# Kernel optimization log

Measured on AMD Instinct MI355X. Metric: run time of the kernel, lower is better.

The kernel has to match this reference:

```python
import jax, jax.numpy as jnp
import numpy as np

D_HEAD = 64  # module's self.heads scaling constant


def setup_inputs() -> dict:
    key = jax.random.key(0)
    kq, kk, kv = jax.random.split(key, 3)
    N, HW, C = 4, 4096, 64
    Q = jax.random.normal(kq, (N, HW, C), dtype=jnp.float32)
    K = jax.random.normal(kk, (N, HW, C), dtype=jnp.float32)
    V = jax.random.normal(kv, (N, HW, C), dtype=jnp.float32)
    return {"Q": Q, "K": K, "V": V}


def reference(Q, K, V):
    # logits[n, q, k] = Q[n,q,:] . K[n,k,:] / sqrt(d_head)
    scale = 1.0 / jnp.sqrt(jnp.asarray(D_HEAD, dtype=Q.dtype))
    logits = jnp.einsum("nqc,nkc->nqk", Q, K) * scale  # [N, HW, HW]
    # NOTE: softmax over the QUERY axis (dim=1), non-standard
    attn = jax.nn.softmax(logits, axis=1)
    return jnp.einsum("nqk,nkc->nqc", attn, V)
```

## Files before the change

kernel.cpp:

```cpp
#include <hip/hip_runtime.h>
#include <hip/hip_bf16.h>

#define NB 4
#define HWN 4096
#define CD 64
#define NSTRIDE (HWN * CD)

typedef short short8 __attribute__((ext_vector_type(8), may_alias));
typedef short short4v __attribute__((ext_vector_type(4), may_alias));
typedef float f32x4 __attribute__((ext_vector_type(4), may_alias));
typedef unsigned int uint4v __attribute__((ext_vector_type(4), may_alias));

__device__ constexpr float C1 = 0.18033688011112042f;

__device__ __forceinline__ unsigned short f2bf(float f) {
    unsigned u = __builtin_bit_cast(unsigned, f);
    u = (u + 0x7FFFu + ((u >> 16) & 1u)) >> 16;
    return (unsigned short)u;
}

__device__ __forceinline__ float fexp2(float x) {
#if __has_builtin(__builtin_amdgcn_exp2f)
    return __builtin_amdgcn_exp2f(x);
#else
    return exp2f(x);
#endif
}

__device__ __forceinline__ unsigned pk2(float a, float b) {
    __hip_bfloat162 h = __float22bfloat162_rn(float2{a, b});
    unsigned u;
    __builtin_memcpy(&u, &h, 4);
    return u;
}

__device__ __forceinline__ size_t qk_swz(int row, int c) {
    return (size_t)(row >> 4) * 1024 + (c >> 5) * 512 +
           ((((c >> 3) & 3) * 16 + (row & 15)) * 8) + (c & 7);
}

__device__ __forceinline__ int k_perm_row(int r) {
    int G = r >> 5, a = r & 31;
    int j = a & 7, g = a >> 3;
    return (G << 5) + ((j >> 2) << 4) + g * 4 + (j & 3);
}

__global__ __launch_bounds__(256) void cvt_qkv(const float* __restrict__ Q,
                                               const float* __restrict__ K,
                                               const float* __restrict__ V,
                                               unsigned short* __restrict__ Qs,
                                               unsigned short* __restrict__ Ks,
                                               unsigned short* __restrict__ Vts,
                                               float* __restrict__ l) {
    __shared__ float tile[64][65];
    int tid = threadIdx.x;
    if (blockIdx.x < 16) {
        int zi = blockIdx.x * 256 + tid;
        *(f32x4*)(l + (size_t)zi * 4) = f32x4{0.f, 0.f, 0.f, 0.f};
    }
    {
        int i = (blockIdx.x * 256 + tid) * 4;
        int rg = i >> 6, c = i & 63;
        int n = rg >> 12, r = rg & 4095;
        float4 q = *(const float4*)(Q + i);
        float4 k = *(const float4*)(K + i);
        ushort4 qo, ko;
        qo.x = f2bf(q.x * C1); qo.y = f2bf(q.y * C1);
        qo.z = f2bf(q.z * C1); qo.w = f2bf(q.w * C1);
        ko.x = f2bf(k.x); ko.y = f2bf(k.y); ko.z = f2bf(k.z); ko.w = f2bf(k.w);
        *(ushort4*)(Qs + (size_t)n * NSTRIDE + qk_swz(r, c)) = qo;
        *(ushort4*)(Ks + (size_t)n * NSTRIDE + qk_swz(k_perm_row(r), c)) = ko;
    }
    if (blockIdx.x >= 256 && blockIdx.x < 512) {
        int bx = blockIdx.x - 256;
        int n = bx >> 6, kbase = (bx & 63) * 64;
#pragma unroll
        for (int i = 0; i < 16; ++i) {
            int e = i * 256 + tid;
            int k = e >> 6, c = e & 63;
            tile[c][k] = V[((size_t)(n * HWN + kbase + k)) * CD + c];
        }
        __syncthreads();
#pragma unroll
        for (int i = 0; i < 2; ++i) {
            int s = i * 256 + tid;
            int kb32 = s >> 8;
            int ct = (s >> 6) & 3;
            int ll = s & 63;
            int cc = ct * 16 + (ll & 15);
            int k0 = kb32 * 32 + ((ll >> 4) & 3) * 8;
            short8 v;
#pragma unroll
            for (int j = 0; j < 8; ++j)
                v[j] = (short)f2bf(tile[cc][k0 + j]);
            size_t off = (size_t)n * NSTRIDE + (size_t)((kbase >> 5) + kb32) * 2048 +
                         ct * 512 + ll * 8;
            *(short8*)(Vts + off) = v;
        }
    }
}

__global__ __attribute__((amdgpu_flat_work_group_size(256, 256), amdgpu_waves_per_eu(2, 4)))
void lsum_kernel(const unsigned short* __restrict__ Qs,
                 const unsigned short* __restrict__ Ks,
                 float* __restrict__ l) {
    int tid = threadIdx.x;
    int w = tid >> 6, lane = tid & 63, quad = lane >> 4, m16 = lane & 15;
    int n = blockIdx.y;
    int kbase = blockIdx.x * 256 + w * 64;

    const unsigned short* Kp = Ks + (size_t)n * NSTRIDE + (kbase >> 4) * 1024 + lane * 8;
    short8 ka0 = *(const short8*)(Kp);
    short8 ka1 = *(const short8*)(Kp + 512);
    short8 kb0 = *(const short8*)(Kp + 1024);
    short8 kb1 = *(const short8*)(Kp + 1536);
    short8 kc0 = *(const short8*)(Kp + 2048);
    short8 kc1 = *(const short8*)(Kp + 2560);
    short8 kd0 = *(const short8*)(Kp + 3072);
    short8 kd1 = *(const short8*)(Kp + 3584);

    const unsigned short* Qp = Qs + (size_t)n * NSTRIDE + blockIdx.z * 16384 + lane * 8;

    short8 qc0 = *(const short8*)(Qp);
    short8 qc1 = *(const short8*)(Qp + 512);
    Qp += 1024;

    float lA[4] = {0.f, 0.f, 0.f, 0.f};
    float lB[4] = {0.f, 0.f, 0.f, 0.f};
    float lC[4] = {0.f, 0.f, 0.f, 0.f};
    float lD[4] = {0.f, 0.f, 0.f, 0.f};
#pragma unroll 2
    for (int qc = 0; qc < 16; ++qc) {
        short8 qn0 = *(const short8*)(Qp);
        short8 qn1 = *(const short8*)(Qp + 512);
        f32x4 a = {0.f, 0.f, 0.f, 0.f}, b = a, c = a, d = a;
        __builtin_amdgcn_s_setprio(1);
        a = __builtin_amdgcn_mfma_f32_16x16x32_bf16(ka0, qc0, a, 0, 0, 0);
        a = __builtin_amdgcn_mfma_f32_16x16x32_bf16(ka1, qc1, a, 0, 0, 0);
        b = __builtin_amdgcn_mfma_f32_16x16x32_bf16(kb0, qc0, b, 0, 0, 0);
        b = __builtin_amdgcn_mfma_f32_16x16x32_bf16(kb1, qc1, b, 0, 0, 0);
        c = __builtin_amdgcn_mfma_f32_16x16x32_bf16(kc0, qc0, c, 0, 0, 0);
        c = __builtin_amdgcn_mfma_f32_16x16x32_bf16(kc1, qc1, c, 0, 0, 0);
        d = __builtin_amdgcn_mfma_f32_16x16x32_bf16(kd0, qc0, d, 0, 0, 0);
        d = __builtin_amdgcn_mfma_f32_16x16x32_bf16(kd1, qc1, d, 0, 0, 0);
        __builtin_amdgcn_s_setprio(0);
#pragma unroll
        for (int r = 0; r < 4; ++r) {
            lA[r] += fexp2(a[r]);
            lB[r] += fexp2(b[r]);
            lC[r] += fexp2(c[r]);
            lD[r] += fexp2(d[r]);
        }
        qc0 = qn0; qc1 = qn1;
        Qp += 1024;
    }
#pragma unroll
    for (int r = 0; r < 4; ++r)
        for (int d1 = 1; d1 < 16; d1 <<= 1) {
            lA[r] += __shfl_xor(lA[r], d1);
            lB[r] += __shfl_xor(lB[r], d1);
            lC[r] += __shfl_xor(lC[r], d1);
            lD[r] += __shfl_xor(lD[r], d1);
        }
    if (m16 == 0) {
        float* lp = l + n * HWN + kbase + quad * 8;
#pragma unroll
        for (int r = 0; r < 4; ++r) {
            atomicAdd(lp + r, lA[r]);
            atomicAdd(lp + 4 + r, lB[r]);
            atomicAdd(lp + 32 + r, lC[r]);
            atomicAdd(lp + 36 + r, lD[r]);
        }
    }
}

__global__ __attribute__((amdgpu_flat_work_group_size(256, 256), amdgpu_waves_per_eu(2, 4)))
void attn_kernel(const unsigned short* __restrict__ Qs,
                 const unsigned short* __restrict__ Ks,
                 const unsigned short* __restrict__ Vts,
                 const float* __restrict__ l,
                 float* __restrict__ partial,
                 int nit) {
    __shared__ float rls[2048];
    int tid = threadIdx.x;
    int w = tid >> 6, lane = tid & 63, quad = lane >> 4, m16 = lane & 15;
    int n = blockIdx.y;
    int qbase = blockIdx.x * 128 + w * 16;

    int kspan = nit * 32;
    int kk0 = blockIdx.z * kspan;
    for (int i = tid; i < kspan; i += 256)
        rls[i] = 1.0f / l[n * HWN + kk0 + i];

    const unsigned short* Qp = Qs + (size_t)n * NSTRIDE + (qbase >> 4) * 1024 + lane * 8;
    short8 qa0 = *(const short8*)(Qp);
    short8 qa1 = *(const short8*)(Qp + 512);
    short8 qb0 = *(const short8*)(Qp + 4096);
    short8 qb1 = *(const short8*)(Qp + 4096 + 512);

    size_t kofs = (size_t)blockIdx.z * (size_t)nit * 2048;
    const unsigned short* Kp = Ks + (size_t)n * NSTRIDE + kofs + lane * 8;
    const unsigned short* Vp = Vts + (size_t)n * NSTRIDE + kofs + lane * 8;

    f32x4 oA[4], oB[4];
#pragma unroll
    for (int ct = 0; ct < 4; ++ct) { oA[ct] = f32x4{0.f, 0.f, 0.f, 0.f}; oB[ct] = oA[ct]; }

    short8 kf00 = *(const short8*)(Kp);
    short8 kf01 = *(const short8*)(Kp + 512);
    short8 kf10 = *(const short8*)(Kp + 1024);
    short8 kf11 = *(const short8*)(Kp + 1536);

    __syncthreads();

#pragma unroll 2
    for (int it = 0; it < nit; ++it) {
        short8 kn00 = *(const short8*)(Kp + 2048);
        short8 kn01 = *(const short8*)(Kp + 2560);
        short8 kn10 = *(const short8*)(Kp + 3072);
        short8 kn11 = *(const short8*)(Kp + 3584);
        short8 vf0 = *(const short8*)(Vp);
        short8 vf1 = *(const short8*)(Vp + 512);
        short8 vf2 = *(const short8*)(Vp + 1024);
        short8 vf3 = *(const short8*)(Vp + 1536);

        f32x4 s00 = {0.f, 0.f, 0.f, 0.f}, s01 = s00, s10 = s00, s11 = s00;
        __builtin_amdgcn_s_setprio(1);
        s00 = __builtin_amdgcn_mfma_f32_16x16x32_bf16(kf00, qa0, s00, 0, 0, 0);
        s00 = __builtin_amdgcn_mfma_f32_16x16x32_bf16(kf01, qa1, s00, 0, 0, 0);
        s01 = __builtin_amdgcn_mfma_f32_16x16x32_bf16(kf10, qa0, s01, 0, 0, 0);
        s01 = __builtin_amdgcn_mfma_f32_16x16x32_bf16(kf11, qa1, s01, 0, 0, 0);
        s10 = __builtin_amdgcn_mfma_f32_16x16x32_bf16(kf00, qb0, s10, 0, 0, 0);
        s10 = __builtin_amdgcn_mfma_f32_16x16x32_bf16(kf01, qb1, s10, 0, 0, 0);
        s11 = __builtin_amdgcn_mfma_f32_16x16x32_bf16(kf10, qb0, s11, 0, 0, 0);
        s11 = __builtin_amdgcn_mfma_f32_16x16x32_bf16(kf11, qb1, s11, 0, 0, 0);
        __builtin_amdgcn_s_setprio(0);

        const float* rlp = rls + it * 32 + quad * 8;
        f32x4 rlo = *(const f32x4*)(rlp);
        f32x4 rhi = *(const f32x4*)(rlp + 4);

        uint4v wa = {pk2(fexp2(s00[0]) * rlo[0], fexp2(s00[1]) * rlo[1]),
                     pk2(fexp2(s00[2]) * rlo[2], fexp2(s00[3]) * rlo[3]),
                     pk2(fexp2(s01[0]) * rhi[0], fexp2(s01[1]) * rhi[1]),
                     pk2(fexp2(s01[2]) * rhi[2], fexp2(s01[3]) * rhi[3])};
        uint4v wb = {pk2(fexp2(s10[0]) * rlo[0], fexp2(s10[1]) * rlo[1]),
                     pk2(fexp2(s10[2]) * rlo[2], fexp2(s10[3]) * rlo[3]),
                     pk2(fexp2(s11[0]) * rhi[0], fexp2(s11[1]) * rhi[1]),
                     pk2(fexp2(s11[2]) * rhi[2], fexp2(s11[3]) * rhi[3])};
        short8 pA = __builtin_bit_cast(short8, wa);
        short8 pB = __builtin_bit_cast(short8, wb);

        __builtin_amdgcn_s_setprio(1);
        oA[0] = __builtin_amdgcn_mfma_f32_16x16x32_bf16(vf0, pA, oA[0], 0, 0, 0);
        oB[0] = __builtin_amdgcn_mfma_f32_16x16x32_bf16(vf0, pB, oB[0], 0, 0, 0);
        oA[1] = __builtin_amdgcn_mfma_f32_16x16x32_bf16(vf1, pA, oA[1], 0, 0, 0);
        oB[1] = __builtin_amdgcn_mfma_f32_16x16x32_bf16(vf1, pB, oB[1], 0, 0, 0);
        oA[2] = __builtin_amdgcn_mfma_f32_16x16x32_bf16(vf2, pA, oA[2], 0, 0, 0);
        oB[2] = __builtin_amdgcn_mfma_f32_16x16x32_bf16(vf2, pB, oB[2], 0, 0, 0);
        oA[3] = __builtin_amdgcn_mfma_f32_16x16x32_bf16(vf3, pA, oA[3], 0, 0, 0);
        oB[3] = __builtin_amdgcn_mfma_f32_16x16x32_bf16(vf3, pB, oB[3], 0, 0, 0);
        __builtin_amdgcn_s_setprio(0);

        kf00 = kn00; kf01 = kn01; kf10 = kn10; kf11 = kn11;
        Kp += 2048;
        Vp += 2048;
    }

    float* ppA = partial + (size_t)blockIdx.z * (NB * HWN * CD) +
                 ((size_t)(n * HWN + qbase + m16)) * CD + quad * 4;
    float* ppB = ppA + (size_t)64 * CD;
#pragma unroll
    for (int ct = 0; ct < 4; ++ct) {
        *(f32x4*)(ppA + ct * 16) = oA[ct];
        *(f32x4*)(ppB + ct * 16) = oB[ct];
    }
}

__global__ __launch_bounds__(256) void reduce_out(const float* __restrict__ p,
                                                  float* __restrict__ out, int ns) {
    int i = (blockIdx.x * 256 + threadIdx.x) * 4;
    f32x4 a = *(const f32x4*)(p + i);
    for (int s = 1; s < ns; ++s)
        a = a + *(const f32x4*)(p + (size_t)s * (NB * HWN * CD) + i);
    *(f32x4*)(out + i) = a;
}

extern "C" void kernel_launch(void* const* d_in, const int* in_sizes, int n_in,
                              void* d_out, int out_size, void* d_ws, size_t ws_size,
                              hipStream_t stream) {
    const float* Q = (const float*)d_in[0];
    const float* K = (const float*)d_in[1];
    const float* V = (const float*)d_in[2];
    float* out = (float*)d_out;

    char* ws = (char*)d_ws;
    unsigned short* Qs  = (unsigned short*)(ws);
    unsigned short* Ks  = (unsigned short*)(ws + (1u << 21));
    unsigned short* Vts = (unsigned short*)(ws + (2u << 21));
    float* l       = (float*)(ws + (3u << 21));
    float* partial = (float*)(ws + (4u << 21));

    size_t base = (size_t)(4u << 21);
    size_t slice = (size_t)NB * HWN * CD * sizeof(float);
    int ns = (ws_size >= base + 8 * slice) ? 8
           : (ws_size >= base + 4 * slice) ? 4 : 2;
    int nit = HWN / ns / 32;

    cvt_qkv<<<1024, 256, 0, stream>>>(Q, K, V, Qs, Ks, Vts, l);
    lsum_kernel<<<dim3(16, NB, 16), 256, 0, stream>>>(Qs, Ks, l);
    attn_kernel<<<dim3(32, NB, ns), 256, 0, stream>>>(Qs, Ks, Vts, l, partial, nit);
    reduce_out<<<1024, 256, 0, stream>>>(partial, out, ns);
}
```

Before: 112.3 us.

## Stage K/V tiles through double-buffered LDS via global_load_lds

Each block now loads a K and V tile per iteration into shared memory once, using direct global-to-LDS loads and double buffering. All four waves then read the tile from LDS, where before each wave loaded it from global memory itself. The aim is to cut redundant global/L2 traffic across the waves. In exchange it adds a block-wide barrier every iteration and reads one tile past the end on the last iteration. There is no explicit wait on the async LDS load, so correctness depends on the barrier draining vmcnt.

New measurement: 112.4 us. No clear change (+0.1%).

```diff
diff --git a/kernel.cpp b/kernel.cpp
--- a/kernel.cpp
+++ b/kernel.cpp
@@ -181,6 +181,8 @@
                  const float* __restrict__ l,
                  float* __restrict__ partial,
                  int nit) {
+    __shared__ unsigned short sK[2][2048];
+    __shared__ unsigned short sV[2][2048];
     __shared__ float rls[2048];
     int tid = threadIdx.x;
     int w = tid >> 6, lane = tid & 63, quad = lane >> 4, m16 = lane & 15;
@@ -198,31 +200,43 @@
     short8 qb0 = *(const short8*)(Qp + 4096);
     short8 qb1 = *(const short8*)(Qp + 4096 + 512);
 
-    size_t kofs = (size_t)blockIdx.z * (size_t)nit * 2048;
-    const unsigned short* Kp = Ks + (size_t)n * NSTRIDE + kofs + lane * 8;
-    const unsigned short* Vp = Vts + (size_t)n * NSTRIDE + kofs + lane * 8;
+    size_t kofs = (size_t)n * NSTRIDE + (size_t)blockIdx.z * (size_t)nit * 2048;
+    const unsigned short* Kg = Ks + kofs;
+    const unsigned short* Vg = Vts + kofs;
+
+    auto stage = [&](int buf, int it) {
+        const unsigned short* kg = Kg + (size_t)it * 2048 + (size_t)tid * 8;
+        const unsigned short* vg = Vg + (size_t)it * 2048 + (size_t)tid * 8;
+        __builtin_amdgcn_global_load_lds(
+            (const __attribute__((address_space(1))) void*)kg,
+            (__attribute__((address_space(3))) void*)(&sK[buf][w * 512]), 16, 0, 0);
+        __builtin_amdgcn_global_load_lds(
+            (const __attribute__((address_space(1))) void*)vg,
+            (__attribute__((address_space(3))) void*)(&sV[buf][w * 512]), 16, 0, 0);
+    };
 
     f32x4 oA[4], oB[4];
 #pragma unroll
     for (int ct = 0; ct < 4; ++ct) { oA[ct] = f32x4{0.f, 0.f, 0.f, 0.f}; oB[ct] = oA[ct]; }
 
-    short8 kf00 = *(const short8*)(Kp);
-    short8 kf01 = *(const short8*)(Kp + 512);
-    short8 kf10 = *(const short8*)(Kp + 1024);
-    short8 kf11 = *(const short8*)(Kp + 1536);
-
+    stage(0, 0);
     __syncthreads();
 
+    int buf = 0;
 #pragma unroll 2
     for (int it = 0; it < nit; ++it) {
-        short8 kn00 = *(const short8*)(Kp + 2048);
-        short8 kn01 = *(const short8*)(Kp + 2560);
-        short8 kn10 = *(const short8*)(Kp + 3072);
-        short8 kn11 = *(const short8*)(Kp + 3584);
-        short8 vf0 = *(const short8*)(Vp);
-        short8 vf1 = *(const short8*)(Vp + 512);
-        short8 vf2 = *(const short8*)(Vp + 1024);
-        short8 vf3 = *(const short8*)(Vp + 1536);
+        stage(buf ^ 1, it + 1);
+
+        const unsigned short* kb = &sK[buf][lane * 8];
+        const unsigned short* vb = &sV[buf][lane * 8];
+        short8 kf00 = *(const short8*)(kb);
+        short8 kf01 = *(const short8*)(kb + 512);
+        short8 kf10 = *(const short8*)(kb + 1024);
+        short8 kf11 = *(const short8*)(kb + 1536);
+        short8 vf0 = *(const short8*)(vb);
+        short8 vf1 = *(const short8*)(vb + 512);
+        short8 vf2 = *(const short8*)(vb + 1024);
+        short8 vf3 = *(const short8*)(vb + 1536);
 
         f32x4 s00 = {0.f, 0.f, 0.f, 0.f}, s01 = s00, s10 = s00, s11 = s00;
         __builtin_amdgcn_s_setprio(1);
@@ -262,9 +276,8 @@
         oB[3] = __builtin_amdgcn_mfma_f32_16x16x32_bf16(vf3, pB, oB[3], 0, 0, 0);
         __builtin_amdgcn_s_setprio(0);
 
-        kf00 = kn00; kf01 = kn01; kf10 = kn10; kf11 = kn11;
-        Kp += 2048;
-        Vp += 2048;
+        __syncthreads();
+        buf ^= 1;
     }
 
     float* ppA = partial + (size_t)blockIdx.z * (NB * HWN * CD) +
```
